# Optimization experiments

Measured on AMD Instinct MI355X. Metric: run time of the kernel, lower is better.

## Reference

```python
import jax, jax.numpy as jnp
import numpy as np

HIDDEN = 50

def setup_inputs() -> dict:
    key = jax.random.key(0)
    ks = jax.random.split(key, 6)
    B, T, F = 4096, 200, 32
    x = jax.random.normal(ks[0], (B, T, F), dtype=jnp.float32)
    # SimpleRNN params (keras defaults: glorot_uniform kernel, orthogonal recurrent, zero bias)
    lim = np.sqrt(6.0 / (F + HIDDEN))
    W = jax.random.uniform(ks[1], (F, HIDDEN), minval=-lim, maxval=lim, dtype=jnp.float32)
    U = jnp.linalg.qr(jax.random.normal(ks[2], (HIDDEN, HIDDEN)))[0].astype(jnp.float32)
    b = jnp.zeros((HIDDEN,), dtype=jnp.float32)
    # Dense head: RandomNormal(stddev=0.01) kernel, zero bias
    Wd = 0.01 * jax.random.normal(ks[3], (HIDDEN, 1), dtype=jnp.float32)
    bd = jnp.zeros((1,), dtype=jnp.float32)
    return {"x": x, "W": W, "U": U, "b": b, "Wd": Wd, "bd": bd}

def reference(x, W, U, b, Wd, bd):
    B = x.shape[0]
    # Precompute input projections for all timesteps in one GEMM: [B,T,H]
    xw = jnp.einsum('btf,fh->bth', x, W) + b
    h0 = jnp.zeros((B, HIDDEN), dtype=x.dtype)

    def step(h, xw_t):
        h_new = jnp.tanh(xw_t + h @ U)
        return h_new, None

    h_last, _ = jax.lax.scan(step, h0, jnp.swapaxes(xw, 0, 1))  # scan over T
    return jax.nn.relu(h_last @ Wd + bd)  # [B, 1]
```

## Files before the change

### kernel.cpp

```cpp
#include <hip/hip_runtime.h>

#define TT 200
#define FF 32
#define HH 50
#define NFULL 12

typedef _Float16 half8 __attribute__((ext_vector_type(8)));
typedef __attribute__((ext_vector_type(4))) float f32x4;
typedef __attribute__((ext_vector_type(4))) unsigned int uint32x4;

__device__ __forceinline__ float fast_tanh(float x) {
    float e = exp2f(2.885390082f * x);
    return fmaf(-2.0f, __builtin_amdgcn_rcpf(e + 1.0f), 1.0f);
}
__device__ __forceinline__ f32x4 mfmah(half8 a, half8 b, f32x4 c) {
    return __builtin_amdgcn_mfma_f32_16x16x32_f16(a, b, c, 0, 0, 0);
}

__device__ __forceinline__ half8 build_wfrag(const float* __restrict__ M, int kbase,
                                             int kmax, int c, bool cv, int g) {
    unsigned u[4];
#pragma unroll
    for (int q = 0; q < 4; ++q) {
        const int k0 = kbase + 8 * g + 2 * q, k1 = k0 + 1;
        _Float16 v0 = (_Float16)((cv && k0 < kmax) ? M[k0 * HH + c] : 0.0f);
        _Float16 v1 = (_Float16)((cv && k1 < kmax) ? M[k1 * HH + c] : 0.0f);
        u[q] = ((unsigned)__builtin_bit_cast(unsigned short, v1) << 16)
             |  __builtin_bit_cast(unsigned short, v0);
    }
    uint32x4 uu = {u[0], u[1], u[2], u[3]};
    return __builtin_bit_cast(half8, uu);
}

__device__ __forceinline__ half8 cvt8(float4 a, float4 b) {
    unsigned u0 = __builtin_bit_cast(unsigned, __builtin_amdgcn_cvt_pkrtz(a.x, a.y));
    unsigned u1 = __builtin_bit_cast(unsigned, __builtin_amdgcn_cvt_pkrtz(a.z, a.w));
    unsigned u2 = __builtin_bit_cast(unsigned, __builtin_amdgcn_cvt_pkrtz(b.x, b.y));
    unsigned u3 = __builtin_bit_cast(unsigned, __builtin_amdgcn_cvt_pkrtz(b.z, b.w));
    uint32x4 uu = {u0, u1, u2, u3};
    return __builtin_bit_cast(half8, uu);
}

__global__
__attribute__((amdgpu_flat_work_group_size(64, 64)))
__attribute__((amdgpu_waves_per_eu(2, 2)))
void rnn_fp16(const float* __restrict__ x, const float* __restrict__ W,
              const float* __restrict__ U, const float* __restrict__ b,
              const float* __restrict__ Wd, const float* __restrict__ bd,
              float* __restrict__ out)
{
    __shared__ float xw[2][16][2][64];
    __shared__ _Float16 hl[2][2][64];

    const int l = threadIdx.x & 63;
    const int r = l & 15;
    const int g = l >> 4;
    const int rl = r & 1;
    const int rb = blockIdx.x * 2;
    const bool gs1 = (g & 1) != 0, gs2 = (g & 2) != 0;
    const int cg = 16 * g + r;

    half8 Wf[4], U0[4], U1[4];
    f32x4 biasv[4];
#pragma unroll
    for (int n = 0; n < 4; ++n) {
        const int c = 16 * n + r;
        const bool cv = (c < HH);
        Wf[n] = build_wfrag(W, 0,  FF, c, cv, g);
        U0[n] = build_wfrag(U, 0,  HH, c, cv, g);
        U1[n] = build_wfrag(U, 32, HH, c, cv, g);
        const float bv = cv ? b[c] : 0.0f;
        biasv[n] = (f32x4){bv, bv, bv, bv};
    }
    const f32x4 kzero = {0.0f, 0.0f, 0.0f, 0.0f};
    const float wd = (cg < HH) ? Wd[cg] : 0.0f;

    const float* x0 = x + (size_t)(rb + 0) * TT * FF;
    const float* x1 = x + (size_t)(rb + 1) * TT * FF;

    float4 r0a, r0b, r1a, r1b;
    auto chunk_load = [&](int cc) {
        int tt = 16 * cc + r; if (tt > TT - 1) tt = TT - 1;
        const float* p0 = x0 + (size_t)tt * FF + 8 * g;
        const float* p1 = x1 + (size_t)tt * FF + 8 * g;
        r0a = *(const float4*)p0; r0b = *(const float4*)(p0 + 4);
        r1a = *(const float4*)p1; r1b = *(const float4*)(p1 + 4);
    };
    auto chunk_compute = [&](int cc) {
        half8 a0 = cvt8(r0a, r0b);
        half8 a1 = cvt8(r1a, r1b);
        const int par = cc & 1;
#pragma unroll
        for (int n = 0; n < 4; ++n) {
            f32x4 c0 = mfmah(a0, Wf[n], biasv[n]);
            f32x4 c1 = mfmah(a1, Wf[n], biasv[n]);
#pragma unroll
            for (int i = 0; i < 4; ++i) {
                xw[par][4 * g + i][0][16 * n + r] = c0[i];
                xw[par][4 * g + i][1][16 * n + r] = c1[i];
            }
        }
    };

    chunk_load(0);
    chunk_compute(0);
    chunk_load(1);
    ((unsigned*)hl)[l] = 0u;
    ((unsigned*)hl)[64 + l] = 0u;

    float hf0 = 0.0f, hf1 = 0.0f;

    auto step_body = [&](int tl, const float* xwp, bool first) {
        const int buf = tl & 1;
        half8 A0, A1;
        if (!first) {
            const _Float16* hp = &hl[buf][rl][0];
            A0 = *(const half8*)(hp + 8 * g);
            A1 = *(const half8*)(hp + 32 + 8 * g);
        }
        f32x4 tot[4];
        if (!first) {
#pragma unroll
            for (int n = 0; n < 4; ++n)
                tot[n] = mfmah(A1, U1[n], mfmah(A0, U0[n], kzero));
        } else {
#pragma unroll
            for (int n = 0; n < 4; ++n) tot[n] = kzero;
        }
        float m0 = gs2 ? (gs1 ? tot[3][0] : tot[2][0]) : (gs1 ? tot[1][0] : tot[0][0]);
        float m1 = gs2 ? (gs1 ? tot[3][1] : tot[2][1]) : (gs1 ? tot[1][1] : tot[0][1]);
        m0 += xwp[tl * 128];
        m1 += xwp[tl * 128 + 64];
        hf0 = fast_tanh(m0);
        hf1 = fast_tanh(m1);
        hl[buf ^ 1][0][cg] = (_Float16)hf0;
        hl[buf ^ 1][1][cg] = (_Float16)hf1;
    };

    for (int c = 0; c < NFULL; ++c) {
        const float* xwp = (c & 1) ? &xw[1][0][0][cg] : &xw[0][0][0][cg];
#pragma unroll
        for (int tl = 0; tl < 16; ++tl) {
            step_body(tl, xwp, (c == 0) & (tl == 0));
            if (tl == 8) {
                chunk_compute(c + 1);
                chunk_load(c + 2);
            }
        }
    }
    {
        const float* xwp = &xw[0][0][0][cg];
#pragma unroll
        for (int tl = 0; tl < 8; ++tl) step_body(tl, xwp, false);
    }

    float p0 = hf0 * wd, p1 = hf1 * wd;
#pragma unroll
    for (int m = 1; m <= 32; m <<= 1) {
        p0 += __shfl_xor(p0, m);
        p1 += __shfl_xor(p1, m);
    }
    if (l == 0) {
        const float bdv = bd[0];
        out[rb + 0] = fmaxf(p0 + bdv, 0.0f);
        out[rb + 1] = fmaxf(p1 + bdv, 0.0f);
    }
}

extern "C" void kernel_launch(void* const* d_in, const int* in_sizes, int n_in,
                              void* d_out, int out_size, void* d_ws, size_t ws_size,
                              hipStream_t stream) {
    const float* x  = (const float*)d_in[0];
    const float* W  = (const float*)d_in[1];
    const float* U  = (const float*)d_in[2];
    const float* b  = (const float*)d_in[3];
    const float* Wd = (const float*)d_in[4];
    const float* bd = (const float*)d_in[5];
    float* out = (float*)d_out;
    const int B = out_size;
    dim3 grid(B / 2), block(64);
    hipLaunchKernelGGL(rnn_fp16, grid, block, 0, stream,
                       x, W, U, b, Wd, bd, out);
    (void)d_ws; (void)ws_size; (void)in_sizes; (void)n_in;
}
```

Measured before the change: 61.69 us.

## Split batch unevenly across 3072 blocks, halve xw chunk to 8 steps, pad LDS

Launches 3072 single-wave blocks, where the first 1024 handle two sequences and the remaining 2048 handle one, instead of 2048 blocks of two. This balances the 2048 uniform waves across the 256 CUs so the tail wave count improves. The input-projection chunk shrinks from 16 to 8 timesteps, which cuts LDS use and allows a waves_per_eu hint of 3-4. The xw rows are padded to 66 floats to avoid bank conflicts. Single-sequence blocks duplicate work on half the MFMA tile, and the grid is hardcoded to B=4096.

```diff
diff --git a/kernel.cpp b/kernel.cpp
--- a/kernel.cpp
+++ b/kernel.cpp
@@ -3,7 +3,8 @@
 #define TT 200
 #define FF 32
 #define HH 50
-#define NFULL 12
+#define NCH 25
+#define XP 66
 
 typedef _Float16 half8 __attribute__((ext_vector_type(8)));
 typedef __attribute__((ext_vector_type(4))) float f32x4;
@@ -43,20 +44,22 @@
 
 __global__
 __attribute__((amdgpu_flat_work_group_size(64, 64)))
-__attribute__((amdgpu_waves_per_eu(2, 2)))
+__attribute__((amdgpu_waves_per_eu(3, 4)))
 void rnn_fp16(const float* __restrict__ x, const float* __restrict__ W,
               const float* __restrict__ U, const float* __restrict__ b,
               const float* __restrict__ Wd, const float* __restrict__ bd,
               float* __restrict__ out)
 {
-    __shared__ float xw[2][16][2][64];
+    __shared__ float xw[2][8][2][XP];
     __shared__ _Float16 hl[2][2][64];
 
     const int l = threadIdx.x & 63;
     const int r = l & 15;
     const int g = l >> 4;
     const int rl = r & 1;
-    const int rb = blockIdx.x * 2;
+    const int bid = blockIdx.x;
+    const bool two = (bid < 1024);
+    const int rb = two ? 2 * bid : bid + 1024;
     const bool gs1 = (g & 1) != 0, gs2 = (g & 2) != 0;
     const int cg = 16 * g + r;
 
@@ -76,11 +79,11 @@
     const float wd = (cg < HH) ? Wd[cg] : 0.0f;
 
     const float* x0 = x + (size_t)(rb + 0) * TT * FF;
-    const float* x1 = x + (size_t)(rb + 1) * TT * FF;
+    const float* x1 = x + (size_t)(rb + (two ? 1 : 0)) * TT * FF;
 
     float4 r0a, r0b, r1a, r1b;
     auto chunk_load = [&](int cc) {
-        int tt = 16 * cc + r; if (tt > TT - 1) tt = TT - 1;
+        int tt = 8 * cc + (r & 7); if (tt > TT - 1) tt = TT - 1;
         const float* p0 = x0 + (size_t)tt * FF + 8 * g;
         const float* p1 = x1 + (size_t)tt * FF + 8 * g;
         r0a = *(const float4*)p0; r0b = *(const float4*)(p0 + 4);
@@ -94,10 +97,12 @@
         for (int n = 0; n < 4; ++n) {
             f32x4 c0 = mfmah(a0, Wf[n], biasv[n]);
             f32x4 c1 = mfmah(a1, Wf[n], biasv[n]);
+            if (g < 2) {
 #pragma unroll
-            for (int i = 0; i < 4; ++i) {
-                xw[par][4 * g + i][0][16 * n + r] = c0[i];
-                xw[par][4 * g + i][1][16 * n + r] = c1[i];
+                for (int i = 0; i < 4; ++i) {
+                    xw[par][4 * g + i][0][16 * n + r] = c0[i];
+                    xw[par][4 * g + i][1][16 * n + r] = c1[i];
+                }
             }
         }
     };
@@ -129,29 +134,24 @@
         }
         float m0 = gs2 ? (gs1 ? tot[3][0] : tot[2][0]) : (gs1 ? tot[1][0] : tot[0][0]);
         float m1 = gs2 ? (gs1 ? tot[3][1] : tot[2][1]) : (gs1 ? tot[1][1] : tot[0][1]);
-        m0 += xwp[tl * 128];
-        m1 += xwp[tl * 128 + 64];
+        m0 += xwp[tl * (2 * XP)];
+        m1 += xwp[tl * (2 * XP) + XP];
         hf0 = fast_tanh(m0);
         hf1 = fast_tanh(m1);
         hl[buf ^ 1][0][cg] = (_Float16)hf0;
         hl[buf ^ 1][1][cg] = (_Float16)hf1;
     };
 
-    for (int c = 0; c < NFULL; ++c) {
+    for (int c = 0; c < NCH; ++c) {
         const float* xwp = (c & 1) ? &xw[1][0][0][cg] : &xw[0][0][0][cg];
 #pragma unroll
-        for (int tl = 0; tl < 16; ++tl) {
+        for (int tl = 0; tl < 8; ++tl) {
             step_body(tl, xwp, (c == 0) & (tl == 0));
-            if (tl == 8) {
+            if (tl == 4 && c + 1 < NCH) {
                 chunk_compute(c + 1);
                 chunk_load(c + 2);
             }
         }
-    }
-    {
-        const float* xwp = &xw[0][0][0][cg];
-#pragma unroll
-        for (int tl = 0; tl < 8; ++tl) step_body(tl, xwp, false);
     }
 
     float p0 = hf0 * wd, p1 = hf1 * wd;
@@ -162,8 +162,8 @@
     }
     if (l == 0) {
         const float bdv = bd[0];
-        out[rb + 0] = fmaxf(p0 + bdv, 0.0f);
-        out[rb + 1] = fmaxf(p1 + bdv, 0.0f);
+        out[rb] = fmaxf(p0 + bdv, 0.0f);
+        if (two) out[rb + 1] = fmaxf(p1 + bdv, 0.0f);
     }
 }
 
@@ -177,9 +177,8 @@
     const float* Wd = (const float*)d_in[4];
     const float* bd = (const float*)d_in[5];
     float* out = (float*)d_out;
-    const int B = out_size;
-    dim3 grid(B / 2), block(64);
+    dim3 grid(3072), block(64);
     hipLaunchKernelGGL(rnn_fp16, grid, block, 0, stream,
                        x, W, U, b, Wd, bd, out);
-    (void)d_ws; (void)ws_size; (void)in_sizes; (void)n_in;
+    (void)d_ws; (void)ws_size; (void)in_sizes; (void)n_in; (void)out_size;
 }
```

After: 90.08 us. +46.0%, slower.

## Spread input-projection MFMA tiles across recurrence steps and pack xw pairs

Applied to the files above, without the earlier changes.

The next-chunk input projection, previously done all at once at step 8, is now split into four per-tile MFMA groups interleaved over steps 5-8. The fp16 conversion moves to step 4 and the global load to step 10. The xw shared buffer becomes float2 pairs with padded rows, so each step reads both batch rows in one LDS load. The hidden-state buffer is padded to 96, so only the first 64 entries get zeroed. The aim is to hide projection work inside the latency-bound serial recurrence and cut LDS instructions, at the cost of more code and a different register live range.

```diff
diff --git a/kernel.cpp b/kernel.cpp
--- a/kernel.cpp
+++ b/kernel.cpp
@@ -4,9 +4,11 @@
 #define FF 32
 #define HH 50
 #define NFULL 12
+#define HLP 96
 
 typedef _Float16 half8 __attribute__((ext_vector_type(8)));
 typedef __attribute__((ext_vector_type(4))) float f32x4;
+typedef __attribute__((ext_vector_type(2))) float f32x2;
 typedef __attribute__((ext_vector_type(4))) unsigned int uint32x4;
 
 __device__ __forceinline__ float fast_tanh(float x) {
@@ -49,8 +51,8 @@
               const float* __restrict__ Wd, const float* __restrict__ bd,
               float* __restrict__ out)
 {
-    __shared__ float xw[2][16][2][64];
-    __shared__ _Float16 hl[2][2][64];
+    __shared__ f32x2 xw[2][16][66];
+    __shared__ _Float16 hl[2][2][HLP];
 
     const int l = threadIdx.x & 63;
     const int r = l & 15;
@@ -79,6 +81,7 @@
     const float* x1 = x + (size_t)(rb + 1) * TT * FF;
 
     float4 r0a, r0b, r1a, r1b;
+    half8 ca0, ca1;
     auto chunk_load = [&](int cc) {
         int tt = 16 * cc + r; if (tt > TT - 1) tt = TT - 1;
         const float* p0 = x0 + (size_t)tt * FF + 8 * g;
@@ -86,31 +89,24 @@
         r0a = *(const float4*)p0; r0b = *(const float4*)(p0 + 4);
         r1a = *(const float4*)p1; r1b = *(const float4*)(p1 + 4);
     };
-    auto chunk_compute = [&](int cc) {
-        half8 a0 = cvt8(r0a, r0b);
-        half8 a1 = cvt8(r1a, r1b);
-        const int par = cc & 1;
+    auto chunk_tile = [&](int par, int n) {
+        f32x4 c0 = mfmah(ca0, Wf[n], biasv[n]);
+        f32x4 c1 = mfmah(ca1, Wf[n], biasv[n]);
 #pragma unroll
-        for (int n = 0; n < 4; ++n) {
-            f32x4 c0 = mfmah(a0, Wf[n], biasv[n]);
-            f32x4 c1 = mfmah(a1, Wf[n], biasv[n]);
-#pragma unroll
-            for (int i = 0; i < 4; ++i) {
-                xw[par][4 * g + i][0][16 * n + r] = c0[i];
-                xw[par][4 * g + i][1][16 * n + r] = c1[i];
-            }
-        }
+        for (int i = 0; i < 4; ++i)
+            xw[par][4 * g + i][16 * n + r] = (f32x2){c0[i], c1[i]};
     };
 
     chunk_load(0);
-    chunk_compute(0);
+    ca0 = cvt8(r0a, r0b); ca1 = cvt8(r1a, r1b);
+    chunk_tile(0, 0); chunk_tile(0, 1); chunk_tile(0, 2); chunk_tile(0, 3);
     chunk_load(1);
-    ((unsigned*)hl)[l] = 0u;
-    ((unsigned*)hl)[64 + l] = 0u;
+    hl[0][0][cg] = (_Float16)0.0f;
+    hl[0][1][cg] = (_Float16)0.0f;
 
     float hf0 = 0.0f, hf1 = 0.0f;
 
-    auto step_body = [&](int tl, const float* xwp, bool first) {
+    auto step_body = [&](int tl, const f32x2* xwp, bool first) {
         const int buf = tl & 1;
         half8 A0, A1;
         if (!first) {
@@ -129,8 +125,9 @@
         }
         float m0 = gs2 ? (gs1 ? tot[3][0] : tot[2][0]) : (gs1 ? tot[1][0] : tot[0][0]);
         float m1 = gs2 ? (gs1 ? tot[3][1] : tot[2][1]) : (gs1 ? tot[1][1] : tot[0][1]);
-        m0 += xwp[tl * 128];
-        m1 += xwp[tl * 128 + 64];
+        const f32x2 xv = xwp[tl * 66];
+        m0 += xv[0];
+        m1 += xv[1];
         hf0 = fast_tanh(m0);
         hf1 = fast_tanh(m1);
         hl[buf ^ 1][0][cg] = (_Float16)hf0;
@@ -138,18 +135,21 @@
     };
 
     for (int c = 0; c < NFULL; ++c) {
-        const float* xwp = (c & 1) ? &xw[1][0][0][cg] : &xw[0][0][0][cg];
+        const f32x2* xwp = (c & 1) ? &xw[1][0][cg] : &xw[0][0][cg];
+        const int npar = (c + 1) & 1;
 #pragma unroll
         for (int tl = 0; tl < 16; ++tl) {
             step_body(tl, xwp, (c == 0) & (tl == 0));
-            if (tl == 8) {
-                chunk_compute(c + 1);
-                chunk_load(c + 2);
-            }
+            if (tl == 4) { ca0 = cvt8(r0a, r0b); ca1 = cvt8(r1a, r1b); }
+            if (tl == 5) chunk_tile(npar, 0);
+            if (tl == 6) chunk_tile(npar, 1);
+            if (tl == 7) chunk_tile(npar, 2);
+            if (tl == 8) chunk_tile(npar, 3);
+            if (tl == 10) chunk_load(c + 2);
         }
     }
     {
-        const float* xwp = &xw[0][0][0][cg];
+        const f32x2* xwp = &xw[0][0][cg];
 #pragma unroll
         for (int tl = 0; tl < 8; ++tl) step_body(tl, xwp, false);
     }
```

Result: slower. 63.07 us (+2.2%).
